# Kernel optimization log

Hardware: AMD Instinct MI355X
Metric: run time of the kernel (lower is better)

Reference implementation:

```python
import jax, jax.numpy as jnp
import numpy as np

SAMPLE_RATE = 48000
FREQ_MIN, FREQ_MAX = 20.0, 2000.0
MOD_MIN, MOD_MAX = -1.0, 2.0


def setup_inputs() -> dict:
    key = jax.random.key(0)
    k1, k2, k3 = jax.random.split(key, 3)
    B, N = 512, 65536
    freq = jax.random.uniform(k1, (B, 1), dtype=jnp.float32)
    mod_env = jax.random.uniform(k2, (B, N), dtype=jnp.float32)
    mod_amount = jax.random.uniform(k3, (B, 1), dtype=jnp.float32)
    return {"num_samples": N, "freq": freq, "mod_env": mod_env, "mod_amount": mod_amount}


def reference(num_samples, freq, mod_env, mod_amount):
    # de-normalize controls
    f0 = FREQ_MIN + (FREQ_MAX - FREQ_MIN) * freq            # [B, 1] Hz
    f0 = 2.0 * jnp.pi * f0 / SAMPLE_RATE                    # [B, 1] rad/sample
    mod_amt = MOD_MIN + (MOD_MAX - MOD_MIN) * mod_amount    # [B, 1]
    # instantaneous angular frequency per sample: f0 * (1 + mod_env * mod_amt)
    freq_env = f0 + mod_env * mod_amt * f0                  # [B, N]
    # prepend zero, cumsum, drop last -> exclusive prefix sum (phase)
    padded = jnp.concatenate([jnp.zeros_like(freq_env[:, :1]), freq_env], axis=-1)
    phase = jnp.cumsum(padded, axis=-1)[:, :-1]             # [B, N]
    return jnp.sin(phase)
```

## Files before the change

### kernel.cpp

```cpp
#include <hip/hip_runtime.h>


constexpr int BLOCK = 1024;
constexpr int VPT   = 8;
constexpr int NW    = BLOCK / 64;
constexpr int WELEM = 64 * VPT;

typedef float f32x4 __attribute__((ext_vector_type(4)));

__global__ __launch_bounds__(BLOCK) void osc_kernel(
    const float* __restrict__ freq,
    const float* __restrict__ mod_env,
    const float* __restrict__ mod_amount,
    float* __restrict__ out,
    int N)
{
    const int row  = blockIdx.x;
    const int tid  = threadIdx.x;
    const int lane = tid & 63;
    const int wid  = tid >> 6;

    __shared__ double s_wsum[2][NW];

    const double f0rev = (20.0 + 1980.0 * (double)freq[row]) / 48000.0;
    const double amt   = -1.0 + 3.0 * (double)mod_amount[row];
    const float  kf    = (float)(f0rev * amt);
    const float  f0f   = (float)f0rev;

    const int chunk  = BLOCK * VPT;
    const int nchunk = N / chunk;

    const float* __restrict__ wload  = mod_env + (size_t)row * N + wid * WELEM + 4 * lane;
    float*       __restrict__ wstore = out     + (size_t)row * N + wid * WELEM + 4 * lane;

    double carry = 0.0;

    f32x4 curA = *(const f32x4*)(wload);
    f32x4 curB = *(const f32x4*)(wload + 256);

    for (int c = 0; c < nchunk; ++c) {
        f32x4 nxtA = curA, nxtB = curB;
        if (c + 1 < nchunk) {
            const float* p = wload + (size_t)(c + 1) * chunk;
            nxtA = *(const f32x4*)(p);
            nxtB = *(const f32x4*)(p + 256);
        }

        float va0 = fmaf(curA.x, kf, f0f), va1 = fmaf(curA.y, kf, f0f);
        float va2 = fmaf(curA.z, kf, f0f), va3 = fmaf(curA.w, kf, f0f);
        float vb0 = fmaf(curB.x, kf, f0f), vb1 = fmaf(curB.y, kf, f0f);
        float vb2 = fmaf(curB.z, kf, f0f), vb3 = fmaf(curB.w, kf, f0f);

        float sa = (va0 + va1) + (va2 + va3);
        float sb = (vb0 + vb1) + (vb2 + vb3);

        double xa = (double)sa, xb = (double)sb;
        #pragma unroll
        for (int off = 1; off < 64; off <<= 1) {
            double ya = __shfl_up(xa, off, 64);
            double yb = __shfl_up(xb, off, 64);
            if (lane >= off) { xa += ya; xb += yb; }
        }
        double Ta = __shfl(xa, 63, 64);

        if (lane == 63) s_wsum[c & 1][wid] = xa + xb;
        __syncthreads();

        double w = (lane < NW) ? s_wsum[c & 1][lane] : 0.0;
        #pragma unroll
        for (int off = 1; off < NW; off <<= 1) {
            double y = __shfl_up(w, off, 64);
            if (lane >= off) w += y;
        }
        double total = __shfl(w, NW - 1, 64);
        double exc   = __shfl(w, (wid > 0 ? wid - 1 : 0), 64);
        if (wid == 0) exc = 0.0;

        double base = carry + exc;
        carry += total;

        double ph0 = base + (xa - (double)sa);
        double ph1 = base + Ta + (xb - (double)sb);

        float bf0 = (float)(ph0 - floor(ph0));
        float bf1 = (float)(ph1 - floor(ph1));

        f32x4 oA, oB;
        {
            float pf, fr;
            pf = bf0;
            fr = pf - floorf(pf); oA.x = __builtin_amdgcn_sinf(fr); pf += va0;
            fr = pf - floorf(pf); oA.y = __builtin_amdgcn_sinf(fr); pf += va1;
            fr = pf - floorf(pf); oA.z = __builtin_amdgcn_sinf(fr); pf += va2;
            fr = pf - floorf(pf); oA.w = __builtin_amdgcn_sinf(fr);
            pf = bf1;
            fr = pf - floorf(pf); oB.x = __builtin_amdgcn_sinf(fr); pf += vb0;
            fr = pf - floorf(pf); oB.y = __builtin_amdgcn_sinf(fr); pf += vb1;
            fr = pf - floorf(pf); oB.z = __builtin_amdgcn_sinf(fr); pf += vb2;
            fr = pf - floorf(pf); oB.w = __builtin_amdgcn_sinf(fr);
        }

        float* q = wstore + (size_t)c * chunk;
        *(f32x4*)(q)       = oA;
        *(f32x4*)(q + 256) = oB;

        curA = nxtA; curB = nxtB;
    }
}

extern "C" void kernel_launch(void* const* d_in, const int* in_sizes, int n_in,
                              void* d_out, int out_size, void* d_ws, size_t ws_size,
                              hipStream_t stream) {
    const float* freq       = (const float*)d_in[1];
    const float* mod_env    = (const float*)d_in[2];
    const float* mod_amount = (const float*)d_in[3];
    float* out = (float*)d_out;

    const int B = in_sizes[1];
    const int N = in_sizes[2] / B;

    osc_kernel<<<B, BLOCK, 0, stream>>>(freq, mod_env, mod_amount, out, N);
}
```

Baseline: 46.08 us.

## Replace per-chunk block barrier with chained wave-to-wave flag handoff in LDS

Removes the __syncthreads and the block-level scan of wave sums in each chunk. Each wave now spins on an LDS flag set by its predecessor wave (or by the last wave of the previous chunk), reads that inclusive total, and publishes its own. This lets fast waves run ahead instead of stalling at a barrier, but it serializes the carry through a chain of spin-waits. It also assumes the chunk count fits in MAXCH=16 (N/8192=8 here), and it can deadlock if waves are not co-resident or are scheduled unfairly.

```diff
diff --git a/kernel.cpp b/kernel.cpp
--- a/kernel.cpp
+++ b/kernel.cpp
@@ -5,6 +5,7 @@
 constexpr int VPT   = 8;
 constexpr int NW    = BLOCK / 64;
 constexpr int WELEM = 64 * VPT;
+constexpr int MAXCH = 16;
 
 typedef float f32x4 __attribute__((ext_vector_type(4)));
 
@@ -20,7 +21,11 @@
     const int lane = tid & 63;
     const int wid  = tid >> 6;
 
-    __shared__ double s_wsum[2][NW];
+    __shared__ double s_tot[MAXCH][NW];
+    __shared__ int    s_flag[MAXCH][NW];
+
+    for (int i = tid; i < MAXCH * NW; i += BLOCK) ((int*)s_flag)[i] = 0;
+    __syncthreads();
 
     const double f0rev = (20.0 + 1980.0 * (double)freq[row]) / 48000.0;
     const double amt   = -1.0 + 3.0 * (double)mod_amount[row];
@@ -32,8 +37,6 @@
 
     const float* __restrict__ wload  = mod_env + (size_t)row * N + wid * WELEM + 4 * lane;
     float*       __restrict__ wstore = out     + (size_t)row * N + wid * WELEM + 4 * lane;
-
-    double carry = 0.0;
 
     f32x4 curA = *(const f32x4*)(wload);
     f32x4 curB = *(const f32x4*)(wload + 256);
@@ -62,25 +65,26 @@
             if (lane >= off) { xa += ya; xb += yb; }
         }
         double Ta = __shfl(xa, 63, 64);
+        double T  = __shfl(xa + xb, 63, 64);
 
-        if (lane == 63) s_wsum[c & 1][wid] = xa + xb;
-        __syncthreads();
+        double E = 0.0;
+        if (!(c == 0 && wid == 0)) {
+            const int pc = (wid == 0) ? c - 1 : c;
+            const int pw = (wid == 0) ? NW - 1 : wid - 1;
+            while (__hip_atomic_load(&s_flag[pc][pw], __ATOMIC_ACQUIRE,
+                                     __HIP_MEMORY_SCOPE_WORKGROUP) == 0) {
+                __builtin_amdgcn_s_sleep(1);
+            }
+            E = s_tot[pc][pw];
+        }
+        if (lane == 0) {
+            s_tot[c][wid] = E + T;
+            __hip_atomic_store(&s_flag[c][wid], 1, __ATOMIC_RELEASE,
+                               __HIP_MEMORY_SCOPE_WORKGROUP);
+        }
 
-        double w = (lane < NW) ? s_wsum[c & 1][lane] : 0.0;
-        #pragma unroll
-        for (int off = 1; off < NW; off <<= 1) {
-            double y = __shfl_up(w, off, 64);
-            if (lane >= off) w += y;
-        }
-        double total = __shfl(w, NW - 1, 64);
-        double exc   = __shfl(w, (wid > 0 ? wid - 1 : 0), 64);
-        if (wid == 0) exc = 0.0;
-
-        double base = carry + exc;
-        carry += total;
-
-        double ph0 = base + (xa - (double)sa);
-        double ph1 = base + Ta + (xb - (double)sb);
+        double ph0 = E + (xa - (double)sa);
+        double ph1 = E + Ta + (xb - (double)sb);
 
         float bf0 = (float)(ph0 - floor(ph0));
         float bf1 = (float)(ph1 - floor(ph1));
```

Result: slower. 48.70 us (+5.7%).
